# Kernel tuning notes

Measured on AMD Instinct MI355X. Metric: run time of the kernel, lower is better.

The kernel has to match this reference:

```python
import jax, jax.numpy as jnp
import numpy as np

ALPHA = 0.2  # LeakyReLU negative slope
NEG = -1e11  # mask value from original code (-100000000000.0)


def _gat_layer(x, adj_mask, W, av1, av2):
    # x: [N, F_in], W: [F_out, F_in], av1/av2: [F_out]
    wh = x @ W.T                                   # [N, F_out]
    wh1 = wh @ av1                                 # [N]
    wh2 = wh @ av2                                 # [N]
    e = wh1[:, None] + wh2[None, :]                # [N, N]
    e = jnp.where(e > 0, e, ALPHA * e)             # LeakyReLU
    att = jnp.where(adj_mask, e, NEG)
    att = jax.nn.softmax(att, axis=-1)
    return att @ wh                                # [N, F_out]


def setup_inputs() -> dict:
    key = jax.random.key(0)
    ks = jax.random.split(key, 8)
    N, F_IN, H, HID, NCLS = 4096, 512, 8, 64, 64
    s = 0.05  # xavier-ish scale
    x = jax.random.normal(ks[0], (N, F_IN), dtype=jnp.float32)
    adj = jax.random.randint(ks[1], (N, N), 0, 2, dtype=jnp.int32)
    W = jax.random.normal(ks[2], (H, HID, F_IN), dtype=jnp.float32) * s
    a1 = jax.random.normal(ks[3], (H, HID), dtype=jnp.float32) * s
    a2 = jax.random.normal(ks[4], (H, HID), dtype=jnp.float32) * s
    W2 = jax.random.normal(ks[5], (NCLS, H * HID), dtype=jnp.float32) * s
    a21 = jax.random.normal(ks[6], (NCLS,), dtype=jnp.float32) * s
    a22 = jax.random.normal(ks[7], (NCLS,), dtype=jnp.float32) * s
    return {"x": x, "adj": adj, "W": W, "a1": a1, "a2": a2,
            "W2": W2, "a21": a21, "a22": a22}


def reference(x, adj, W, a1, a2, W2, a21, a22):
    adj_mask = adj > 0                              # [N, N] bool
    # multi-head layers (concat=True -> ELU per head, concat on feature dim)
    heads = jax.vmap(_gat_layer, in_axes=(None, None, 0, 0, 0))(
        x, adj_mask, W, a1, a2)                     # [H, N, HID]
    heads = jax.nn.elu(heads)
    N = x.shape[0]
    h = jnp.transpose(heads, (1, 0, 2)).reshape(N, -1)  # [N, H*HID]
    # last layer (concat=False), then outer ELU + log_softmax
    out = _gat_layer(h, adj_mask, W2, a21, a22)     # [N, NCLS]
    out = jax.nn.elu(out)
    return jax.nn.log_softmax(out, axis=1)
```

## Files before the change

### kernel.cpp

```cpp
#include <hip/hip_runtime.h>

#define Nn 4096
#define FIN 512
#define NH 8
#define O1 512
#define LOG2E 1.44269504088896f

typedef __attribute__((ext_vector_type(8))) short short8;
typedef __attribute__((ext_vector_type(4))) float f32x4;
typedef __attribute__((ext_vector_type(2))) unsigned int u32x2;

__device__ __forceinline__ unsigned short f2bf(float f){
  union{float f; unsigned u;} x; x.f=f;
  unsigned r = x.u + 0x7fffu + ((x.u>>16)&1u);
  return (unsigned short)(r>>16);
}
__device__ __forceinline__ float bf2f(unsigned short b){
  union{unsigned u; float f;} x; x.u=((unsigned)b)<<16;
  return x.f;
}
__device__ __forceinline__ unsigned cvtpk_bf16(float a, float b){
  unsigned r; asm("v_cvt_pk_bf16_f32 %0, %1, %2" : "=v"(r) : "v"(a), "v"(b));
  return r;
}
__device__ __forceinline__ void gload_lds16(const unsigned short* g, unsigned short* l){
  __builtin_amdgcn_global_load_lds(
      (const __attribute__((address_space(1))) unsigned int*)g,
      (__attribute__((address_space(3))) unsigned int*)l, 16, 0, 0);
}

__global__ void k_pack_adj(const int* __restrict__ adj, unsigned long long* __restrict__ adjw){
  size_t tid = (size_t)blockIdx.x*blockDim.x + threadIdx.x;
  int v = __builtin_nontemporal_load(adj + tid);
  unsigned long long m = __ballot(v>0);
  if((threadIdx.x&63)==0) adjw[tid>>6] = m;
}

__global__ void k_cvt_all(const float* __restrict__ x, const float* __restrict__ W,
                          const float* __restrict__ W2,
                          unsigned short* __restrict__ xb, unsigned short* __restrict__ Wb,
                          unsigned short* __restrict__ W2b){
  const int NX = Nn*FIN, NW = O1*FIN, NW2 = 64*FIN;
  int i = (blockIdx.x*blockDim.x + threadIdx.x)*4;
  const float* src; unsigned short* dst; int off;
  if (i < NX){ src=x; dst=xb; off=i; }
  else if (i < NX+NW){ src=W; dst=Wb; off=i-NX; }
  else if (i < NX+NW+NW2){ src=W2; dst=W2b; off=i-NX-NW; }
  else return;
  float4 v = *(const float4*)(src+off);
  u32x2 pk; pk.x = cvtpk_bf16(v.x, v.y); pk.y = cvtpk_bf16(v.z, v.w);
  *(u32x2*)(dst+off) = pk;
}

template<int NWC, int KS>
__global__ __launch_bounds__(NWC*KS*64, 2)
void k_gemm3(const unsigned short* __restrict__ A, const unsigned short* __restrict__ B,
             unsigned short* __restrict__ CT, int M, int K, int O){
  int t=threadIdx.x, l=t&63, w=t>>6;
  int wc=w%NWC, ks=w/NWC;
  int m0=blockIdx.x*32, o0=blockIdx.y*(NWC*32);
  int row=l&15, kq=(l>>4)*8, g=l>>4;
  int kw=K/KS;
  const unsigned short* Ab = A + (size_t)(m0+row)*K + ks*kw + kq;
  const unsigned short* Bb = B + (size_t)(o0+wc*32+row)*K + ks*kw + kq;
  f32x4 acc[2][2]={};
  #pragma unroll 2
  for(int k0=0;k0<kw;k0+=32){
    short8 a0=*(const short8*)(Ab+k0);
    short8 a1=*(const short8*)(Ab+(size_t)16*K+k0);
    short8 b0=*(const short8*)(Bb+k0);
    short8 b1=*(const short8*)(Bb+(size_t)16*K+k0);
    acc[0][0]=__builtin_amdgcn_mfma_f32_16x16x32_bf16(a0,b0,acc[0][0],0,0,0);
    acc[0][1]=__builtin_amdgcn_mfma_f32_16x16x32_bf16(a0,b1,acc[0][1],0,0,0);
    acc[1][0]=__builtin_amdgcn_mfma_f32_16x16x32_bf16(a1,b0,acc[1][0],0,0,0);
    acc[1][1]=__builtin_amdgcn_mfma_f32_16x16x32_bf16(a1,b1,acc[1][1],0,0,0);
  }
  __shared__ float red[NWC][KS/2][32][36];
  for(int s=KS/2;s>=1;s>>=1){
    if(ks>=s && ks<2*s){
      #pragma unroll
      for(int mi=0;mi<2;mi++)
      #pragma unroll
      for(int oi=0;oi<2;oi++)
      #pragma unroll
      for(int r=0;r<4;r++)
        red[wc][ks-s][mi*16+g*4+r][oi*18+row]=acc[mi][oi][r];
    }
    __syncthreads();
    if(ks<s){
      #pragma unroll
      for(int mi=0;mi<2;mi++)
      #pragma unroll
      for(int oi=0;oi<2;oi++)
      #pragma unroll
      for(int r=0;r<4;r++)
        acc[mi][oi][r]+=red[wc][ks][mi*16+g*4+r][oi*18+row];
    }
    __syncthreads();
  }
  if(ks==0){
    #pragma unroll
    for(int mi=0;mi<2;mi++)
    #pragma unroll
    for(int oi=0;oi<2;oi++){
      int m=m0+mi*16+g*4;
      int o=o0+wc*32+oi*16+row;
      u32x2 pk;
      pk.x=cvtpk_bf16(acc[mi][oi][0], acc[mi][oi][1]);
      pk.y=cvtpk_bf16(acc[mi][oi][2], acc[mi][oi][3]);
      *(u32x2*)&CT[(size_t)o*M+m] = pk;
    }
  }
}

__global__ void k_wh12(const unsigned short* __restrict__ whT,
                       const float* __restrict__ a1, const float* __restrict__ a2,
                       float2* __restrict__ e1f1, float* __restrict__ E2a,
                       float* __restrict__ F2a){
  const int M=Nn;
  int n=blockIdx.x*blockDim.x+threadIdx.x;
  int h=blockIdx.y;
  float s1=0.f,s2=0.f;
  for(int c=0;c<64;c++){
    float v=bf2f(whT[(size_t)(h*64+c)*M+n]);
    s1+=v*a1[h*64+c];
    s2+=v*a2[h*64+c];
  }
  float s1L=s1*LOG2E, s2L=s2*LOG2E;
  float2 r1; r1.x=__builtin_amdgcn_exp2f(s1L); r1.y=__builtin_amdgcn_exp2f(0.2f*s1L);
  e1f1[(size_t)h*M+n]=r1;
  E2a[(size_t)h*M+n]=__builtin_amdgcn_exp2f(s2L);
  F2a[(size_t)h*M+n]=__builtin_amdgcn_exp2f(0.2f*s2L);
}

template<int JSTEPS, int LOGH, int JCLOG, int FINAL>
__global__ __launch_bounds__(256, 2)
void k_attn10(const unsigned long long* __restrict__ adjw,
              const float2* __restrict__ e1f1, const float* __restrict__ E2a,
              const float* __restrict__ F2a,
              const unsigned short* __restrict__ whT,
              unsigned short* __restrict__ Hmat,
              unsigned short* __restrict__ Opart, float* __restrict__ Dpart){
  const int M = Nn;
  __shared__ unsigned short buf[2][4][64][64];
  int t = threadIdx.x, l = t & 63, w = t >> 6;
  int rw = w & 1, jw = w >> 1;
  int lr = l & 15, g = l >> 4;
  int bid = blockIdx.x;
  int h = bid & ((1<<LOGH)-1);
  int bx = bid >> LOGH;
  int jc = bx & ((1<<JCLOG)-1);
  int rowtile = bx >> JCLOG;
  int i_base = rowtile*64 + rw*32;
  int jbase = jc*(2*JSTEPS*64) + jw*(JSTEPS*64);
  const float* E2h = E2a + (size_t)h*M;
  const float* F2h = F2a + (size_t)h*M;
  const unsigned short* Vb = whT + (size_t)h*64*M;

  float E1[2], F1[2];
  const unsigned long long* arow[2];
  #pragma unroll
  for (int rf=0; rf<2; rf++){
    int i = i_base + rf*16 + lr;
    float2 ef = e1f1[(size_t)h*M + i];
    E1[rf]=ef.x; F1[rf]=ef.y;
    arow[rf] = adjw + (size_t)i*64;
  }

  const unsigned short* vsrc[4];
  #pragma unroll
  for (int k=0;k<4;k++){
    int rloc = rw*32 + k*8 + (l>>3);
    vsrc[k] = Vb + (size_t)rloc*M + jbase + (((l&7)^(rloc&7))<<3);
  }

  short8 ones;
  #pragma unroll
  for (int q=0;q<8;q++) ones[q] = (short)0x3F80;

  f32x4 acc[2][4] = {};
  f32x4 accd[2] = {};

  #define STAGE(nb, s) do{ \
      gload_lds16(vsrc[0] + (size_t)(s)*64, &buf[jw][nb][rw*32   ][0]); \
      gload_lds16(vsrc[1] + (size_t)(s)*64, &buf[jw][nb][rw*32+ 8][0]); \
      gload_lds16(vsrc[2] + (size_t)(s)*64, &buf[jw][nb][rw*32+16][0]); \
      gload_lds16(vsrc[3] + (size_t)(s)*64, &buf[jw][nb][rw*32+24][0]); \
    }while(0)

  STAGE(0, 0);
  if (1 < JSTEPS) STAGE(1, 1);
  if (2 < JSTEPS) STAGE(2, 2);
  f32x4 eS[2][2], fS[2][2];
  unsigned long long wrd[2];
  #pragma unroll
  for (int half=0; half<2; half++){
    int j = jbase + half*32 + g*8;
    eS[half][0] = *(const f32x4*)(E2h + j);
    eS[half][1] = *(const f32x4*)(E2h + j + 4);
    fS[half][0] = *(const f32x4*)(F2h + j);
    fS[half][1] = *(const f32x4*)(F2h + j + 4);
  }
  wrd[0] = arow[0][jbase>>6];
  wrd[1] = arow[1][jbase>>6];
  asm volatile("s_waitcnt vmcnt(8)" ::: "memory");
  __builtin_amdgcn_sched_barrier(0);
  __builtin_amdgcn_s_barrier();

  for (int s = 0; s < JSTEPS; s++){
    if (s+3 < JSTEPS) STAGE((s+3)&3, s+3);
    unsigned pu[2][2][4];
    #pragma unroll
    for (int half = 0; half < 2; half++){
      #pragma unroll
      for (int rf = 0; rf < 2; rf++){
        unsigned bits = (unsigned)(wrd[rf] >> (half*32 + g*8)) & 0xffu;
        float pf[8];
        #pragma unroll
        for (int q = 0; q < 8; q++){
          float Ev = (q<4) ? eS[half][0][q&3] : eS[half][1][q&3];
          float Fv = (q<4) ? fS[half][0][q&3] : fS[half][1][q&3];
          float m = E1[rf]*Ev;
          float f = F1[rf]*Fv;
          float p = fmaxf(m, f);
          int mk = (int)(bits << (31-q)) >> 31;
          pf[q] = __uint_as_float(__float_as_uint(p) & (unsigned)mk);
        }
        #pragma unroll
        for (int k = 0; k < 4; k++) pu[rf][half][k] = cvtpk_bf16(pf[2*k], pf[2*k+1]);
      }
    }
    if (s+1 < JSTEPS){
      int jn = jbase + (s+1)*64;
      #pragma unroll
      for (int half=0; half<2; half++){
        int j = jn + half*32 + g*8;
        eS[half][0] = *(const f32x4*)(E2h + j);
        eS[half][1] = *(const f32x4*)(E2h + j + 4);
        fS[half][0] = *(const f32x4*)(F2h + j);
        fS[half][1] = *(const f32x4*)(F2h + j + 4);
      }
      wrd[0] = arow[0][jn>>6];
      wrd[1] = arow[1][jn>>6];
    }
    #pragma unroll
    for (int half = 0; half < 2; half++){
      short8 bfr[4];
      #pragma unroll
      for (int ct = 0; ct < 4; ct++)
        bfr[ct] = *(const short8*)&buf[jw][s&3][ct*16+lr][(((half*4+g)^(lr&7))<<3)];
      #pragma unroll
      for (int rf = 0; rf < 2; rf++){
        union { unsigned u[4]; short8 v; } pv_;
        #pragma unroll
        for (int k = 0; k < 4; k++) pv_.u[k] = pu[rf][half][k];
        #pragma unroll
        for (int ct = 0; ct < 4; ct++)
          acc[rf][ct] = __builtin_amdgcn_mfma_f32_16x16x32_bf16(pv_.v, bfr[ct], acc[rf][ct], 0,0,0);
        accd[rf] = __builtin_amdgcn_mfma_f32_16x16x32_bf16(pv_.v, ones, accd[rf], 0,0,0);
      }
    }
    __builtin_amdgcn_s_barrier();
  }
  #undef STAGE

  float* cmb  = (float*)&buf[0][0][0][0];
  float* cmbD = cmb + 64*65;
  __syncthreads();
  if (jw == 1){
    #pragma unroll
    for (int rf=0; rf<2; rf++){
      #pragma unroll
      for (int ct=0; ct<4; ct++)
        #pragma unroll
        for (int r=0; r<4; r++)
          cmb[(rw*32 + rf*16 + g*4 + r)*65 + ct*16 + lr] = acc[rf][ct][r];
      if (lr == 0){
        #pragma unroll
        for (int r=0; r<4; r++)
          cmbD[rw*32 + rf*16 + g*4 + r] = accd[rf][r];
      }
    }
  }
  __syncthreads();
  if (jw == 0){
    #pragma unroll
    for (int rf=0; rf<2; rf++){
      #pragma unroll
      for (int r=0; r<4; r++){
        int rloc = rw*32 + rf*16 + g*4 + r;
        float d = accd[rf][r] + cmbD[rloc];
        float rd = 1.f / fmaxf(d, 1e-30f);
        int row = rowtile*64 + rloc;
        if (FINAL){
          size_t pbase = (size_t)jc*Nn + row;
          if (lr == 0) Dpart[pbase] = d;
          #pragma unroll
          for (int ct=0; ct<4; ct++){
            float v = acc[rf][ct][r] + cmb[rloc*65 + ct*16 + lr];
            Opart[pbase*64 + ct*16 + lr] = f2bf(v);
          }
        } else {
          #pragma unroll
          for (int ct=0; ct<4; ct++){
            float v = (acc[rf][ct][r] + cmb[rloc*65 + ct*16 + lr]) * rd;
            v = v > 0.f ? v : __expf(v) - 1.f;
            Hmat[(size_t)row*O1 + h*64 + ct*16 + lr] = f2bf(v);
          }
        }
      }
    }
  }
}

__global__ void k_fin2(const unsigned short* __restrict__ Op, const float* __restrict__ Dp,
                       float* __restrict__ out){
  int w = threadIdx.x>>6, l = threadIdx.x&63;
  int row = blockIdx.x*4 + w;
  float o = 0.f, d = 0.f;
  #pragma unroll
  for (int jc=0; jc<8; jc++){
    o += bf2f(Op[((size_t)jc*Nn + row)*64 + l]);
    d += Dp[(size_t)jc*Nn + row];
  }
  float v = o / fmaxf(d, 1e-30f);
  v = v > 0.f ? v : __expf(v) - 1.f;
  float m = v;
  #pragma unroll
  for (int dd=1; dd<64; dd<<=1) m = fmaxf(m, __shfl_xor(m, dd));
  float s = __expf(v - m);
  #pragma unroll
  for (int dd=1; dd<64; dd<<=1) s += __shfl_xor(s, dd);
  out[(size_t)row*64 + l] = v - (m + __logf(s));
}

extern "C" void kernel_launch(void* const* d_in, const int* in_sizes, int n_in,
                              void* d_out, int out_size, void* d_ws, size_t ws_size,
                              hipStream_t stream){
  const float* x  = (const float*)d_in[0];
  const int* adj  = (const int*)d_in[1];
  const float* W  = (const float*)d_in[2];
  const float* a1 = (const float*)d_in[3];
  const float* a2 = (const float*)d_in[4];
  const float* W2 = (const float*)d_in[5];
  const float* a21= (const float*)d_in[6];
  const float* a22= (const float*)d_in[7];
  float* out = (float*)d_out;
  char* ws = (char*)d_ws;

  size_t off=0;
  unsigned long long* adjw = (unsigned long long*)(ws+off); off += (size_t)Nn*64*8;
  unsigned short* xb   = (unsigned short*)(ws+off); off += (size_t)Nn*FIN*2;
  unsigned short* Wb   = (unsigned short*)(ws+off); off += (size_t)O1*FIN*2;
  unsigned short* W2b  = (unsigned short*)(ws+off); off += (size_t)64*FIN*2;
  unsigned short* whT1 = (unsigned short*)(ws+off); off += (size_t)O1*Nn*2;
  unsigned short* Hmat = (unsigned short*)(ws+off); off += (size_t)Nn*O1*2;
  unsigned short* whT2 = (unsigned short*)(ws+off); off += (size_t)64*Nn*2;
  float2* e1f1a = (float2*)(ws+off); off += (size_t)NH*Nn*8;
  float*  E2aa  = (float*)(ws+off); off += (size_t)NH*Nn*4;
  float*  F2aa  = (float*)(ws+off); off += (size_t)NH*Nn*4;
  float2* e1f1b = (float2*)(ws+off); off += (size_t)Nn*8;
  float*  E2ab  = (float*)(ws+off); off += (size_t)Nn*4;
  float*  F2ab  = (float*)(ws+off); off += (size_t)Nn*4;
  unsigned short* Opart = (unsigned short*)(ws+off); off += (size_t)8*Nn*64*2;
  float* Dpart = (float*)(ws+off); off += (size_t)8*Nn*4;

  k_pack_adj<<<(Nn*(size_t)Nn)/256, 256, 0, stream>>>(adj, adjw);
  {
    int tot = (Nn*FIN + O1*FIN + 64*FIN)/4;
    k_cvt_all<<<(tot+255)/256, 256, 0, stream>>>(x, W, W2, xb, Wb, W2b);
  }
  k_gemm3<2,4><<<dim3(Nn/32, O1/64), 512, 0, stream>>>(xb, Wb, whT1, Nn, FIN, O1);
  k_wh12<<<dim3(Nn/256, NH), 256, 0, stream>>>(whT1, a1, a2, e1f1a, E2aa, F2aa);
  k_attn10<32, 3, 0, 0><<<(Nn/64)*NH, 256, 0, stream>>>(adjw, e1f1a, E2aa, F2aa, whT1, Hmat, nullptr, nullptr);
  k_gemm3<2,8><<<dim3(Nn/32, 1), 1024, 0, stream>>>(Hmat, W2b, whT2, Nn, FIN, 64);
  k_wh12<<<dim3(Nn/256, 1), 256, 0, stream>>>(whT2, a21, a22, e1f1b, E2ab, F2ab);
  k_attn10<4, 0, 3, 1><<<(Nn/64)*8, 256, 0, stream>>>(adjw, e1f1b, E2ab, F2ab, whT2, nullptr, Opart, Dpart);
  k_fin2<<<Nn/4, 256, 0, stream>>>(Opart, Dpart, out);
  (void)in_sizes; (void)n_in; (void)out_size; (void)ws_size;
}
```

Before: 134.9 us.

## Switch pipeline to fp16 and compute attention weights with packed half math

Replaces bf16 storage and MFMAs with fp16 throughout: the GEMMs, the whT and Hmat buffers, and the E2/F2 exponent tables. In the attention kernel, the masked LeakyReLU-exp weights are now built with packed v_pk_mul/v_pk_max f16 ops and pair masks, instead of per-element fp32 math followed by bf16 conversion. The E2/F2 tables are prefetched into LDS with global_load_lds, and the j-loop is unrolled by four with the adjacency words prefetched. This is meant to cut VALU work and global traffic in the attention inner loop. It adds a risk of fp16 range or rounding problems in the exponent products.

```diff
diff --git a/kernel.cpp b/kernel.cpp
--- a/kernel.cpp
+++ b/kernel.cpp
@@ -6,9 +6,11 @@
 #define O1 512
 #define LOG2E 1.44269504088896f
 
-typedef __attribute__((ext_vector_type(8))) short short8;
+typedef __attribute__((ext_vector_type(8))) _Float16 half8;
+typedef __attribute__((ext_vector_type(2))) _Float16 h2;
 typedef __attribute__((ext_vector_type(4))) float f32x4;
 typedef __attribute__((ext_vector_type(2))) unsigned int u32x2;
+typedef unsigned long long ull;
 
 __device__ __forceinline__ unsigned short f2bf(float f){
   union{float f; unsigned u;} x; x.f=f;
@@ -19,9 +21,18 @@
   union{unsigned u; float f;} x; x.u=((unsigned)b)<<16;
   return x.f;
 }
-__device__ __forceinline__ unsigned cvtpk_bf16(float a, float b){
-  unsigned r; asm("v_cvt_pk_bf16_f32 %0, %1, %2" : "=v"(r) : "v"(a), "v"(b));
-  return r;
+__device__ __forceinline__ h2 pkrtz(float a, float b){
+  return __builtin_bit_cast(h2, __builtin_amdgcn_cvt_pkrtz(a, b));
+}
+__device__ __forceinline__ h2 pkmul(h2 a, h2 b){
+  h2 r; asm("v_pk_mul_f16 %0,%1,%2":"=v"(r):"v"(a),"v"(b)); return r;
+}
+__device__ __forceinline__ h2 pkmax(h2 a, h2 b){
+  h2 r; asm("v_pk_max_f16 %0,%1,%2":"=v"(r):"v"(a),"v"(b)); return r;
+}
+__device__ __forceinline__ unsigned pairmask(unsigned bits, int k){
+  unsigned s = ((bits >> (2*k)) * 0x8001u) & 0x10001u;
+  return s * 0xFFFFu;
 }
 __device__ __forceinline__ void gload_lds16(const unsigned short* g, unsigned short* l){
   __builtin_amdgcn_global_load_lds(
@@ -29,10 +40,10 @@
       (__attribute__((address_space(3))) unsigned int*)l, 16, 0, 0);
 }
 
-__global__ void k_pack_adj(const int* __restrict__ adj, unsigned long long* __restrict__ adjw){
+__global__ void k_pack_adj(const int* __restrict__ adj, ull* __restrict__ adjw){
   size_t tid = (size_t)blockIdx.x*blockDim.x + threadIdx.x;
   int v = __builtin_nontemporal_load(adj + tid);
-  unsigned long long m = __ballot(v>0);
+  ull m = __ballot(v>0);
   if((threadIdx.x&63)==0) adjw[tid>>6] = m;
 }
 
@@ -48,7 +59,9 @@
   else if (i < NX+NW+NW2){ src=W2; dst=W2b; off=i-NX-NW; }
   else return;
   float4 v = *(const float4*)(src+off);
-  u32x2 pk; pk.x = cvtpk_bf16(v.x, v.y); pk.y = cvtpk_bf16(v.z, v.w);
+  h2 lo = pkrtz(v.x, v.y);
+  h2 hi = pkrtz(v.z, v.w);
+  u32x2 pk; pk.x = __builtin_bit_cast(unsigned, lo); pk.y = __builtin_bit_cast(unsigned, hi);
   *(u32x2*)(dst+off) = pk;
 }
 
@@ -66,14 +79,14 @@
   f32x4 acc[2][2]={};
   #pragma unroll 2
   for(int k0=0;k0<kw;k0+=32){
-    short8 a0=*(const short8*)(Ab+k0);
-    short8 a1=*(const short8*)(Ab+(size_t)16*K+k0);
-    short8 b0=*(const short8*)(Bb+k0);
-    short8 b1=*(const short8*)(Bb+(size_t)16*K+k0);
-    acc[0][0]=__builtin_amdgcn_mfma_f32_16x16x32_bf16(a0,b0,acc[0][0],0,0,0);
-    acc[0][1]=__builtin_amdgcn_mfma_f32_16x16x32_bf16(a0,b1,acc[0][1],0,0,0);
-    acc[1][0]=__builtin_amdgcn_mfma_f32_16x16x32_bf16(a1,b0,acc[1][0],0,0,0);
-    acc[1][1]=__builtin_amdgcn_mfma_f32_16x16x32_bf16(a1,b1,acc[1][1],0,0,0);
+    half8 a0=*(const half8*)(Ab+k0);
+    half8 a1=*(const half8*)(Ab+(size_t)16*K+k0);
+    half8 b0=*(const half8*)(Bb+k0);
+    half8 b1=*(const half8*)(Bb+(size_t)16*K+k0);
+    acc[0][0]=__builtin_amdgcn_mfma_f32_16x16x32_f16(a0,b0,acc[0][0],0,0,0);
+    acc[0][1]=__builtin_amdgcn_mfma_f32_16x16x32_f16(a0,b1,acc[0][1],0,0,0);
+    acc[1][0]=__builtin_amdgcn_mfma_f32_16x16x32_f16(a1,b0,acc[1][0],0,0,0);
+    acc[1][1]=__builtin_amdgcn_mfma_f32_16x16x32_f16(a1,b1,acc[1][1],0,0,0);
   }
   __shared__ float red[NWC][KS/2][32][36];
   for(int s=KS/2;s>=1;s>>=1){
@@ -105,9 +118,9 @@
     for(int oi=0;oi<2;oi++){
       int m=m0+mi*16+g*4;
       int o=o0+wc*32+oi*16+row;
-      u32x2 pk;
-      pk.x=cvtpk_bf16(acc[mi][oi][0], acc[mi][oi][1]);
-      pk.y=cvtpk_bf16(acc[mi][oi][2], acc[mi][oi][3]);
+      h2 lo = pkrtz(acc[mi][oi][0], acc[mi][oi][1]);
+      h2 hi = pkrtz(acc[mi][oi][2], acc[mi][oi][3]);
+      u32x2 pk; pk.x=__builtin_bit_cast(unsigned, lo); pk.y=__builtin_bit_cast(unsigned, hi);
       *(u32x2*)&CT[(size_t)o*M+m] = pk;
     }
   }
@@ -115,34 +128,36 @@
 
 __global__ void k_wh12(const unsigned short* __restrict__ whT,
                        const float* __restrict__ a1, const float* __restrict__ a2,
-                       float2* __restrict__ e1f1, float* __restrict__ E2a,
-                       float* __restrict__ F2a){
+                       float2* __restrict__ e1f1, unsigned short* __restrict__ E2a,
+                       unsigned short* __restrict__ F2a){
   const int M=Nn;
   int n=blockIdx.x*blockDim.x+threadIdx.x;
   int h=blockIdx.y;
   float s1=0.f,s2=0.f;
   for(int c=0;c<64;c++){
-    float v=bf2f(whT[(size_t)(h*64+c)*M+n]);
+    float v=(float)__builtin_bit_cast(_Float16, whT[(size_t)(h*64+c)*M+n]);
     s1+=v*a1[h*64+c];
     s2+=v*a2[h*64+c];
   }
   float s1L=s1*LOG2E, s2L=s2*LOG2E;
   float2 r1; r1.x=__builtin_amdgcn_exp2f(s1L); r1.y=__builtin_amdgcn_exp2f(0.2f*s1L);
   e1f1[(size_t)h*M+n]=r1;
-  E2a[(size_t)h*M+n]=__builtin_amdgcn_exp2f(s2L);
-  F2a[(size_t)h*M+n]=__builtin_amdgcn_exp2f(0.2f*s2L);
+  E2a[(size_t)h*M+n]=__builtin_bit_cast(unsigned short,(_Float16)__builtin_amdgcn_exp2f(s2L));
+  F2a[(size_t)h*M+n]=__builtin_bit_cast(unsigned short,(_Float16)__builtin_amdgcn_exp2f(0.2f*s2L));
 }
 
 template<int JSTEPS, int LOGH, int JCLOG, int FINAL>
 __global__ __launch_bounds__(256, 2)
-void k_attn10(const unsigned long long* __restrict__ adjw,
-              const float2* __restrict__ e1f1, const float* __restrict__ E2a,
-              const float* __restrict__ F2a,
+void k_attn11(const ull* __restrict__ adjw,
+              const float2* __restrict__ e1f1,
+              const unsigned short* __restrict__ E2a,
+              const unsigned short* __restrict__ F2a,
               const unsigned short* __restrict__ whT,
               unsigned short* __restrict__ Hmat,
               unsigned short* __restrict__ Opart, float* __restrict__ Dpart){
   const int M = Nn;
-  __shared__ unsigned short buf[2][4][64][64];
+  __shared__ __align__(16) unsigned short vbuf[2][4][64][64];
+  __shared__ __align__(16) unsigned short efbuf[2][2][JSTEPS*64];
   int t = threadIdx.x, l = t & 63, w = t >> 6;
   int rw = w & 1, jw = w >> 1;
   int lr = l & 15, g = l >> 4;
@@ -153,118 +168,121 @@
   int rowtile = bx >> JCLOG;
   int i_base = rowtile*64 + rw*32;
   int jbase = jc*(2*JSTEPS*64) + jw*(JSTEPS*64);
-  const float* E2h = E2a + (size_t)h*M;
-  const float* F2h = F2a + (size_t)h*M;
   const unsigned short* Vb = whT + (size_t)h*64*M;
 
-  float E1[2], F1[2];
-  const unsigned long long* arow[2];
-  #pragma unroll
-  for (int rf=0; rf<2; rf++){
-    int i = i_base + rf*16 + lr;
-    float2 ef = e1f1[(size_t)h*M + i];
-    E1[rf]=ef.x; F1[rf]=ef.y;
-    arow[rf] = adjw + (size_t)i*64;
-  }
-
-  const unsigned short* vsrc[4];
+  h2 E1h[2], F1h[2];
+  const ull *ar0, *ar1;
+  {
+    int i0 = i_base + lr, i1 = i_base + 16 + lr;
+    float2 a = e1f1[(size_t)h*M + i0];
+    float2 b = e1f1[(size_t)h*M + i1];
+    E1h[0] = pkrtz(a.x, a.x);
+    F1h[0] = pkrtz(a.y, a.y);
+    E1h[1] = pkrtz(b.x, b.x);
+    F1h[1] = pkrtz(b.y, b.y);
+    ar0 = adjw + (size_t)i0*64 + (jbase>>6);
+    ar1 = adjw + (size_t)i1*64 + (jbase>>6);
+  }
+
+  const unsigned short* vs[4];
   #pragma unroll
   for (int k=0;k<4;k++){
     int rloc = rw*32 + k*8 + (l>>3);
-    vsrc[k] = Vb + (size_t)rloc*M + jbase + (((l&7)^(rloc&7))<<3);
-  }
-
-  short8 ones;
+    vs[k] = Vb + (size_t)rloc*M + jbase + (((l&7)^(rloc&7))<<3);
+  }
+
+  {
+    const unsigned short* src = (rw ? F2a : E2a) + (size_t)h*M + jbase;
+    unsigned short* dst = &efbuf[jw][rw][0];
+    constexpr int PB = JSTEPS*128;
+    constexpr int NB = (PB + 1023)/1024;
+    #pragma unroll
+    for (int b=0;b<NB;b++){
+      if (b*1024 + l*16 < PB)
+        gload_lds16(src + b*512 + l*8, dst + b*512);
+    }
+  }
+
+  half8 ones;
   #pragma unroll
-  for (int q=0;q<8;q++) ones[q] = (short)0x3F80;
+  for (int q=0;q<8;q++) ones[q] = (_Float16)1.0f;
 
   f32x4 acc[2][4] = {};
   f32x4 accd[2] = {};
 
-  #define STAGE(nb, s) do{ \
-      gload_lds16(vsrc[0] + (size_t)(s)*64, &buf[jw][nb][rw*32   ][0]); \
-      gload_lds16(vsrc[1] + (size_t)(s)*64, &buf[jw][nb][rw*32+ 8][0]); \
-      gload_lds16(vsrc[2] + (size_t)(s)*64, &buf[jw][nb][rw*32+16][0]); \
-      gload_lds16(vsrc[3] + (size_t)(s)*64, &buf[jw][nb][rw*32+24][0]); \
+  #define STAGEV(slot, off) do{ \
+      gload_lds16(vs[0] + (off)*64, &vbuf[jw][slot][rw*32   ][0]); \
+      gload_lds16(vs[1] + (off)*64, &vbuf[jw][slot][rw*32+ 8][0]); \
+      gload_lds16(vs[2] + (off)*64, &vbuf[jw][slot][rw*32+16][0]); \
+      gload_lds16(vs[3] + (off)*64, &vbuf[jw][slot][rw*32+24][0]); \
     }while(0)
 
-  STAGE(0, 0);
-  if (1 < JSTEPS) STAGE(1, 1);
-  if (2 < JSTEPS) STAGE(2, 2);
-  f32x4 eS[2][2], fS[2][2];
-  unsigned long long wrd[2];
-  #pragma unroll
-  for (int half=0; half<2; half++){
-    int j = jbase + half*32 + g*8;
-    eS[half][0] = *(const f32x4*)(E2h + j);
-    eS[half][1] = *(const f32x4*)(E2h + j + 4);
-    fS[half][0] = *(const f32x4*)(F2h + j);
-    fS[half][1] = *(const f32x4*)(F2h + j + 4);
-  }
-  wrd[0] = arow[0][jbase>>6];
-  wrd[1] = arow[1][jbase>>6];
-  asm volatile("s_waitcnt vmcnt(8)" ::: "memory");
+  STAGEV(0,0);
+  if (1 < JSTEPS) STAGEV(1,1);
+  if (2 < JSTEPS) STAGEV(2,2);
+  ull w0 = ar0[0], w1 = ar1[0];
+  asm volatile("s_waitcnt vmcnt(0)" ::: "memory");
   __builtin_amdgcn_sched_barrier(0);
   __builtin_amdgcn_s_barrier();
 
-  for (int s = 0; s < JSTEPS; s++){
-    if (s+3 < JSTEPS) STAGE((s+3)&3, s+3);
-    unsigned pu[2][2][4];
-    #pragma unroll
-    for (int half = 0; half < 2; half++){
-      #pragma unroll
-      for (int rf = 0; rf < 2; rf++){
-        unsigned bits = (unsigned)(wrd[rf] >> (half*32 + g*8)) & 0xffu;
-        float pf[8];
+  const unsigned short* efE = &efbuf[jw][0][g*8];
+  const unsigned short* efF = &efbuf[jw][1][g*8];
+
+  for (int s0 = 0; s0 < JSTEPS; s0 += 4){
+    #pragma unroll
+    for (int u = 0; u < 4; u++){
+      int s = s0 + u;
+      ull wn0=0, wn1=0;
+      if (s+1 < JSTEPS){ wn0 = ar0[u+1]; wn1 = ar1[u+1]; }
+      if (s+3 < JSTEPS) STAGEV((u+3)&3, u+3);
+      union { f32x4 f; h2 hh[4]; } Ee[2], Ff[2];
+      #pragma unroll
+      for (int half=0; half<2; half++){
+        Ee[half].f = *(const f32x4*)(efE + u*64 + half*32);
+        Ff[half].f = *(const f32x4*)(efF + u*64 + half*32);
+      }
+      unsigned pu[2][2][4];
+      #pragma unroll
+      for (int half=0; half<2; half++){
+        unsigned bits0 = (unsigned)(w0 >> (half*32 + g*8)) & 0xffu;
+        unsigned bits1 = (unsigned)(w1 >> (half*32 + g*8)) & 0xffu;
         #pragma unroll
-        for (int q = 0; q < 8; q++){
-          float Ev = (q<4) ? eS[half][0][q&3] : eS[half][1][q&3];
-          float Fv = (q<4) ? fS[half][0][q&3] : fS[half][1][q&3];
-          float m = E1[rf]*Ev;
-          float f = F1[rf]*Fv;
-          float p = fmaxf(m, f);
-          int mk = (int)(bits << (31-q)) >> 31;
-          pf[q] = __uint_as_float(__float_as_uint(p) & (unsigned)mk);
+        for (int k=0;k<4;k++){
+          h2 e2 = Ee[half].hh[k], f2v = Ff[half].hh[k];
+          h2 p0 = pkmax(pkmul(E1h[0], e2), pkmul(F1h[0], f2v));
+          h2 p1 = pkmax(pkmul(E1h[1], e2), pkmul(F1h[1], f2v));
+          pu[0][half][k] = __builtin_bit_cast(unsigned, p0) & pairmask(bits0,k);
+          pu[1][half][k] = __builtin_bit_cast(unsigned, p1) & pairmask(bits1,k);
         }
+      }
+      #pragma unroll
+      for (int half=0; half<2; half++){
+        half8 bfr[4];
         #pragma unroll
-        for (int k = 0; k < 4; k++) pu[rf][half][k] = cvtpk_bf16(pf[2*k], pf[2*k+1]);
+        for (int ct=0; ct<4; ct++)
+          bfr[ct] = *(const half8*)&vbuf[jw][u][ct*16+lr][(((half*4+g)^(lr&7))<<3)];
+        #pragma unroll
+        for (int rf=0; rf<2; rf++){
+          union { unsigned uu[4]; half8 v; } pv_;
+          #pragma unroll
+          for (int k=0;k<4;k++) pv_.uu[k] = pu[rf][half][k];
+          #pragma unroll
+          for (int ct=0; ct<4; ct++)
+            acc[rf][ct] = __builtin_amdgcn_mfma_f32_16x16x32_f16(pv_.v, bfr[ct], acc[rf][ct], 0,0,0);
+          accd[rf] = __builtin_amdgcn_mfma_f32_16x16x32_f16(pv_.v, ones, accd[rf], 0,0,0);
+        }
       }
-    }
-    if (s+1 < JSTEPS){
-      int jn = jbase + (s+1)*64;
-      #pragma unroll
-      for (int half=0; half<2; half++){
-        int j = jn + half*32 + g*8;
-        eS[half][0] = *(const f32x4*)(E2h + j);
-        eS[half][1] = *(const f32x4*)(E2h + j + 4);
-        fS[half][0] = *(const f32x4*)(F2h + j);
-        fS[half][1] = *(const f32x4*)(F2h + j + 4);
-      }
-      wrd[0] = arow[0][jn>>6];
-      wrd[1] = arow[1][jn>>6];
-    }
-    #pragma unroll
-    for (int half = 0; half < 2; half++){
-      short8 bfr[4];
-      #pragma unroll
-      for (int ct = 0; ct < 4; ct++)
-        bfr[ct] = *(const short8*)&buf[jw][s&3][ct*16+lr][(((half*4+g)^(lr&7))<<3)];
-      #pragma unroll
-      for (int rf = 0; rf < 2; rf++){
-        union { unsigned u[4]; short8 v; } pv_;
-        #pragma unroll
-        for (int k = 0; k < 4; k++) pv_.u[k] = pu[rf][half][k];
-        #pragma unroll
-        for (int ct = 0; ct < 4; ct++)
-          acc[rf][ct] = __builtin_amdgcn_mfma_f32_16x16x32_bf16(pv_.v, bfr[ct], acc[rf][ct], 0,0,0);
-        accd[rf] = __builtin_amdgcn_mfma_f32_16x16x32_bf16(pv_.v, ones, accd[rf], 0,0,0);
-      }
-    }
-    __builtin_amdgcn_s_barrier();
-  }
-  #undef STAGE
-
-  float* cmb  = (float*)&buf[0][0][0][0];
+      if (s+1 < JSTEPS){ w0 = wn0; w1 = wn1; }
+      __builtin_amdgcn_s_barrier();
+    }
+    #pragma unroll
+    for (int k=0;k<4;k++) vs[k] += 256;
+    ar0 += 4; ar1 += 4;
+    efE += 256; efF += 256;
+  }
+  #undef STAGEV
+
+  float* cmb  = (float*)&vbuf[0][0][0][0];
   float* cmbD = cmb + 64*65;
   __syncthreads();
   if (jw == 1){
@@ -305,7 +323,8 @@
           for (int ct=0; ct<4; ct++){
             float v = (acc[rf][ct][r] + cmb[rloc*65 + ct*16 + lr]) * rd;
             v = v > 0.f ? v : __expf(v) - 1.f;
-            Hmat[(size_t)row*O1 + h*64 + ct*16 + lr] = f2bf(v);
+            Hmat[(size_t)row*O1 + h*64 + ct*16 + lr] =
+                __builtin_bit_cast(unsigned short, (_Float16)v);
           }
         }
       }
@@ -349,7 +368,7 @@
   char* ws = (char*)d_ws;
 
   size_t off=0;
-  unsigned long long* adjw = (unsigned long long*)(ws+off); off += (size_t)Nn*64*8;
+  ull* adjw = (ull*)(ws+off); off += (size_t)Nn*64*8;
   unsigned short* xb   = (unsigned short*)(ws+off); off += (size_t)Nn*FIN*2;
   unsigned short* Wb   = (unsigned short*)(ws+off); off += (size_t)O1*FIN*2;
   unsigned short* W2b  = (unsigned short*)(ws+off); off += (size_t)64*FIN*2;
@@ -357,11 +376,11 @@
   unsigned short* Hmat = (unsigned short*)(ws+off); off += (size_t)Nn*O1*2;
   unsigned short* whT2 = (unsigned short*)(ws+off); off += (size_t)64*Nn*2;
   float2* e1f1a = (float2*)(ws+off); off += (size_t)NH*Nn*8;
-  float*  E2aa  = (float*)(ws+off); off += (size_t)NH*Nn*4;
-  float*  F2aa  = (float*)(ws+off); off += (size_t)NH*Nn*4;
+  unsigned short* E2aa = (unsigned short*)(ws+off); off += (size_t)NH*Nn*2;
+  unsigned short* F2aa = (unsigned short*)(ws+off); off += (size_t)NH*Nn*2;
   float2* e1f1b = (float2*)(ws+off); off += (size_t)Nn*8;
-  float*  E2ab  = (float*)(ws+off); off += (size_t)Nn*4;
-  float*  F2ab  = (float*)(ws+off); off += (size_t)Nn*4;
+  unsigned short* E2ab = (unsigned short*)(ws+off); off += (size_t)Nn*2;
+  unsigned short* F2ab = (unsigned short*)(ws+off); off += (size_t)Nn*2;
   unsigned short* Opart = (unsigned short*)(ws+off); off += (size_t)8*Nn*64*2;
   float* Dpart = (float*)(ws+off); off += (size_t)8*Nn*4;
 
@@ -372,10 +391,10 @@
   }
   k_gemm3<2,4><<<dim3(Nn/32, O1/64), 512, 0, stream>>>(xb, Wb, whT1, Nn, FIN, O1);
   k_wh12<<<dim3(Nn/256, NH), 256, 0, stream>>>(whT1, a1, a2, e1f1a, E2aa, F2aa);
-  k_attn10<32, 3, 0, 0><<<(Nn/64)*NH, 256, 0, stream>>>(adjw, e1f1a, E2aa, F2aa, whT1, Hmat, nullptr, nullptr);
+  k_attn11<32, 3, 0, 0><<<(Nn/64)*NH, 256, 0, stream>>>(adjw, e1f1a, E2aa, F2aa, whT1, Hmat, nullptr, nullptr);
   k_gemm3<2,8><<<dim3(Nn/32, 1), 1024, 0, stream>>>(Hmat, W2b, whT2, Nn, FIN, 64);
   k_wh12<<<dim3(Nn/256, 1), 256, 0, stream>>>(whT2, a21, a22, e1f1b, E2ab, F2ab);
-  k_attn10<4, 0, 3, 1><<<(Nn/64)*8, 256, 0, stream>>>(adjw, e1f1b, E2ab, F2ab, whT2, nullptr, Opart, Dpart);
+  k_attn11<4, 0, 3, 1><<<(Nn/64)*8, 256, 0, stream>>>(adjw, e1f1b, E2ab, F2ab, whT2, nullptr, Opart, Dpart);
   k_fin2<<<Nn/4, 256, 0, stream>>>(Opart, Dpart, out);
   (void)in_sizes; (void)n_in; (void)out_size; (void)ws_size;
 }
```

Result: faster. 126.8 us (-6.0%).
